# Kernel tuning notes

Hardware: AMD Instinct MI355X
Metric: run time of the kernel (lower is better)

## Reference

```python
import jax, jax.numpy as jnp
import numpy as np

B, S, H, DK = 4, 2048, 16, 64
D = H * DK  # d_model = 1024


def setup_inputs() -> dict:
    key = jax.random.key(0)
    ks = jax.random.split(key, 11)
    s = 1.0 / np.sqrt(D)
    return {
        "query": jax.random.normal(ks[0], (B, S, D), dtype=jnp.float32),
        "value": jax.random.normal(ks[1], (B, S, D), dtype=jnp.float32),
        "key": jax.random.normal(ks[2], (B, S, D), dtype=jnp.float32),
        "Wq": jax.random.normal(ks[3], (D, D), dtype=jnp.float32) * s,
        "bq": jnp.zeros((D,), dtype=jnp.float32),
        "Wk": jax.random.normal(ks[4], (D, D), dtype=jnp.float32) * s,
        "bk": jnp.zeros((D,), dtype=jnp.float32),
        "Wv": jax.random.normal(ks[5], (D, D), dtype=jnp.float32) * s,
        "bv": jnp.zeros((D,), dtype=jnp.float32),
        "Wo": jax.random.normal(ks[6], (D, D), dtype=jnp.float32) * s,
        "bo": jnp.zeros((D,), dtype=jnp.float32),
    }


def _split_heads(x):
    # [B, S, D] -> [B, H, S, DK]
    return x.reshape(B, -1, H, DK).transpose(0, 2, 1, 3)


def reference(query, value, key, Wq, bq, Wk, bk, Wv, bv, Wo, bo):
    q = _split_heads(query @ Wq + bq)
    k = _split_heads(key @ Wk + bk)
    v = _split_heads(value @ Wv + bv)
    logits = jnp.einsum("bhqd,bhkd->bhqk", q, k) / jnp.sqrt(jnp.float32(DK))
    attn = jax.nn.softmax(logits, axis=-1)
    out = jnp.einsum("bhqk,bhkd->bhqd", attn, v)  # [B, H, S, DK]
    out = out.transpose(0, 2, 1, 3).reshape(B, -1, D)
    return out @ Wo + bo
```

## Files before the change

### kernel.cpp

```cpp
#include <hip/hip_runtime.h>

typedef unsigned short u16;
typedef __attribute__((ext_vector_type(4))) short short4v;
typedef __attribute__((ext_vector_type(8))) short short8;
typedef __attribute__((ext_vector_type(4))) float f32x4;

#define MB_ (1024 * 1024)

__device__ __forceinline__ u16 f2bf(float f) {
  union { float f; unsigned int u; } v; v.f = f;
  unsigned int r = (v.u + 0x7FFFu + ((v.u >> 16) & 1u)) >> 16;
  return (u16)r;
}

__device__ __forceinline__ unsigned int pkbf(float a, float b) {
  union { float f; unsigned int u; } x, y; x.f = a; y.f = b;
  return __builtin_amdgcn_perm(y.u + 0x8000u, x.u + 0x8000u, 0x07060302u);
}

__device__ __forceinline__ void async16(const void* g, void* l) {
  __builtin_amdgcn_global_load_lds((__attribute__((address_space(1))) void*)g,
                                   (__attribute__((address_space(3))) void*)l, 16, 0, 0);
}

__device__ __forceinline__ f32x4 mfma32(short8 a, short8 b, f32x4 c) {
  return __builtin_amdgcn_mfma_f32_16x16x32_bf16(a, b, c, 0, 0, 0);
}

__global__ void cvt_x(const float* __restrict__ a, const float* __restrict__ b,
                      const float* __restrict__ c, u16* __restrict__ oa,
                      u16* __restrict__ ob, u16* __restrict__ oc) {
  const float* s = blockIdx.y == 0 ? a : (blockIdx.y == 1 ? b : c);
  u16* d = blockIdx.y == 0 ? oa : (blockIdx.y == 1 ? ob : oc);
  size_t i = ((size_t)blockIdx.x * 256 + threadIdx.x) * 4;
  float4 f = *(const float4*)&s[i];
  ushort4 o;
  o.x = f2bf(f.x); o.y = f2bf(f.y); o.z = f2bf(f.z); o.w = f2bf(f.w);
  *(ushort4*)&d[i] = o;
}

__global__ void wtrans(const float* __restrict__ w0, const float* __restrict__ w1,
                       const float* __restrict__ w2, const float* __restrict__ w3,
                       u16* __restrict__ o0, u16* __restrict__ o1,
                       u16* __restrict__ o2, u16* __restrict__ o3) {
  const int z = blockIdx.z;
  const float* in = z == 0 ? w0 : (z == 1 ? w1 : (z == 2 ? w2 : w3));
  u16* out = z == 0 ? o0 : (z == 1 ? o1 : (z == 2 ? o2 : o3));
  __shared__ float tile[32][33];
  const int bx = blockIdx.x * 32, by = blockIdx.y * 32;
  for (int i = threadIdx.y; i < 32; i += 8)
    tile[i][threadIdx.x] = in[(size_t)(by + i) * 1024 + bx + threadIdx.x];
  __syncthreads();
  for (int i = threadIdx.y; i < 32; i += 8)
    out[(size_t)(bx + i) * 1024 + by + threadIdx.x] = f2bf(tile[threadIdx.x][i]);
}

__device__ __forceinline__ void gemm_body(const u16* __restrict__ A, const u16* __restrict__ Bt,
                                          const float* __restrict__ bias, float alpha,
                                          int mode, void* __restrict__ outp) {
  __shared__ __align__(16) u16 As[128 * 32];
  __shared__ __align__(16) u16 Bs[128 * 32];
  const int t = threadIdx.x, wave = t >> 6, lane = t & 63;
  const int m0 = blockIdx.y * 128, n0 = blockIdx.x * 128;
  const int wm = (wave >> 1) * 64, wn = (wave & 1) * 64;
  const int lrow = lane >> 2, lcol = (lane & 3) * 8;
  f32x4 acc[4][4] = {};
  for (int k0 = 0; k0 < 1024; k0 += 32) {
    __syncthreads();
#pragma unroll
    for (int c = 0; c < 2; ++c) {
      const int chunk = wave * 2 + c;
      const int row = chunk * 16 + lrow;
      async16(&A[(size_t)(m0 + row) * 1024 + k0 + lcol], &As[chunk * 512]);
      async16(&Bt[(size_t)(n0 + row) * 1024 + k0 + lcol], &Bs[chunk * 512]);
    }
    __syncthreads();
    short8 af[4], bf[4];
#pragma unroll
    for (int mb = 0; mb < 4; ++mb)
      af[mb] = *(const short8*)&As[(wm + mb * 16 + (lane & 15)) * 32 + (lane >> 4) * 8];
#pragma unroll
    for (int nb = 0; nb < 4; ++nb)
      bf[nb] = *(const short8*)&Bs[(wn + nb * 16 + (lane & 15)) * 32 + (lane >> 4) * 8];
#pragma unroll
    for (int mb = 0; mb < 4; ++mb)
#pragma unroll
      for (int nb = 0; nb < 4; ++nb)
        acc[mb][nb] = mfma32(af[mb], bf[nb], acc[mb][nb]);
  }
#pragma unroll
  for (int mb = 0; mb < 4; ++mb)
#pragma unroll
    for (int nb = 0; nb < 4; ++nb) {
      const int n = n0 + wn + nb * 16 + (lane & 15);
      const float bn = bias[n];
      if (mode == 2) {
        const int h = n >> 6, d = n & 63;
        const int mbase = m0 + wm + mb * 16 + (lane >> 4) * 4;
        const int b = mbase >> 11, s = mbase & 2047;
        union { unsigned int u[2]; ushort4 s4; } pk;
        pk.u[0] = pkbf(acc[mb][nb][0] + bn, acc[mb][nb][1] + bn);
        pk.u[1] = pkbf(acc[mb][nb][2] + bn, acc[mb][nb][3] + bn);
        *(ushort4*)&((u16*)outp)[(size_t)((b * 16 + h) * 64 + d) * 2048 + s] = pk.s4;
      } else if (mode == 1) {
#pragma unroll
        for (int r = 0; r < 4; ++r) {
          const int m = m0 + wm + mb * 16 + (lane >> 4) * 4 + r;
          const int b = m >> 11, s = m & 2047, h = n >> 6, d = n & 63;
          ((u16*)outp)[(size_t)((b * 16 + h) * 2048 + s) * 64 + d] =
              f2bf(acc[mb][nb][r] * alpha + bn * alpha);
        }
      } else {
#pragma unroll
        for (int r = 0; r < 4; ++r) {
          const int m = m0 + wm + mb * 16 + (lane >> 4) * 4 + r;
          ((float*)outp)[(size_t)m * 1024 + n] = acc[mb][nb][r] + bn;
        }
      }
    }
}

__global__ __launch_bounds__(256, 3) void gemm_proj(
    const u16* xq, const u16* xk, const u16* xv,
    const u16* wq, const u16* wk, const u16* wv,
    const float* bq, const float* bk, const float* bv,
    u16* oq, u16* ok, u16* ov, float aq) {
  const int z = blockIdx.z;
  const u16* A = z == 0 ? xq : (z == 1 ? xk : xv);
  const u16* B = z == 0 ? wq : (z == 1 ? wk : wv);
  const float* bi = z == 0 ? bq : (z == 1 ? bk : bv);
  void* o = z == 0 ? (void*)oq : (z == 1 ? (void*)ok : (void*)ov);
  gemm_body(A, B, bi, z == 0 ? aq : 1.0f, z == 2 ? 2 : 1, o);
}

__global__ __launch_bounds__(256, 3) void gemm_out(const u16* A, const u16* Bt,
                                                   const float* bias, float* o) {
  gemm_body(A, Bt, bias, 1.0f, 0, o);
}

__global__ __launch_bounds__(256, 4) void flash_attn(const u16* __restrict__ Q,
                                                     const u16* __restrict__ K,
                                                     const u16* __restrict__ Vt,
                                                     u16* __restrict__ O) {
  __shared__ __align__(16) u16 lds[2 * 64 * 64];
  u16* Ks = lds;
  u16* Vs = lds + 4096;
  const int t = threadIdx.x, wave = t >> 6, lane = t & 63;
  const int quad = lane >> 4, q15 = lane & 15, sw = q15 & 7;
  const int bh = blockIdx.y, q0 = blockIdx.x * 64;
  const u16* Qb = Q + (size_t)bh * 2048 * 64;
  const u16* Kb = K + (size_t)bh * 2048 * 64;
  const u16* Vb = Vt + (size_t)bh * 64 * 2048;
  const int qr = q0 + wave * 16 + q15;
  const short8 qf0 = *(const short8*)&Qb[(size_t)qr * 64 + quad * 8];
  const short8 qf1 = *(const short8*)&Qb[(size_t)qr * 64 + 32 + quad * 8];
  f32x4 oacc[4] = {};
  float l = 0.f;
  for (int kc = 0; kc < 2048; kc += 64) {
    __syncthreads();
#pragma unroll
    for (int c = 0; c < 2; ++c) {
      const int i = wave * 2 + c;
      const int row = i * 8 + (lane >> 3);
      const int ch = (lane & 7) ^ (row & 7);
      async16(&Kb[(size_t)(kc + row) * 64 + ch * 8], &Ks[i * 512]);
      async16(&Vb[(size_t)row * 2048 + kc + ch * 8], &Vs[i * 512]);
    }
    __syncthreads();
    short4v pk[4];
#pragma unroll
    for (int ma = 0; ma < 4; ++ma) {
      const int rowo = (ma * 16 + q15) * 64;
      const short8 k0 = *(const short8*)&Ks[rowo + ((quad ^ sw) * 8)];
      const short8 k1 = *(const short8*)&Ks[rowo + (((4 + quad) ^ sw) * 8)];
      f32x4 s0 = {};
      s0 = mfma32(k0, qf0, s0);
      s0 = mfma32(k1, qf1, s0);
      float p0 = __builtin_exp2f(s0[0]);
      float p1 = __builtin_exp2f(s0[1]);
      float p2 = __builtin_exp2f(s0[2]);
      float p3 = __builtin_exp2f(s0[3]);
      l += (p0 + p1) + (p2 + p3);
      union { unsigned int u[2]; short4v s4; } pq;
      pq.u[0] = pkbf(p0, p1);
      pq.u[1] = pkbf(p2, p3);
      pk[ma] = pq.s4;
    }
#if __has_builtin(__builtin_amdgcn_mfma_f32_16x16x16bf16_1k)
#pragma unroll
    for (int mb = 0; mb < 4; ++mb) {
      const int vrow = (mb * 16 + q15) * 64;
#pragma unroll
      for (int kb = 0; kb < 4; ++kb) {
        const int pos = (((kb * 2 + (quad >> 1)) ^ sw) * 8) + (quad & 1) * 4;
        const short4v vf = *(const short4v*)&Vs[vrow + pos];
        oacc[mb] = __builtin_amdgcn_mfma_f32_16x16x16bf16_1k(vf, pk[kb], oacc[mb], 0, 0, 0);
      }
    }
#else
    {
      const int* pi = (const int*)&pk[0];
#pragma unroll
      for (int kb2 = 0; kb2 < 2; ++kb2) {
        const int lo = quad < 2 ? pi[kb2 * 4 + 0] : pi[kb2 * 4 + 2];
        const int hi = quad < 2 ? pi[kb2 * 4 + 1] : pi[kb2 * 4 + 3];
        const int src = (2 * (quad & 1)) * 16 + q15;
        union { int i[4]; short8 s; } u;
        u.i[0] = __shfl(lo, src);      u.i[1] = __shfl(hi, src);
        u.i[2] = __shfl(lo, src + 16); u.i[3] = __shfl(hi, src + 16);
#pragma unroll
        for (int mb = 0; mb < 4; ++mb) {
          const short8 vf8 = *(const short8*)&Vs[(mb * 16 + q15) * 64 + (((kb2 * 4 + quad) ^ sw) * 8)];
          oacc[mb] = mfma32(vf8, u.s, oacc[mb]);
        }
      }
    }
#endif
  }
  l += __shfl_xor(l, 16);
  l += __shfl_xor(l, 32);
  const float inv = 1.f / l;
  __syncthreads();
  u16* Es = lds + wave * 1024;
#pragma unroll
  for (int mb = 0; mb < 4; ++mb) {
    const int posc = ((mb * 2 + (quad >> 1)) ^ sw) * 8 + (quad & 1) * 4;
    union { unsigned int u[2]; ushort4 s4; } pq;
    pq.u[0] = pkbf(oacc[mb][0] * inv, oacc[mb][1] * inv);
    pq.u[1] = pkbf(oacc[mb][2] * inv, oacc[mb][3] * inv);
    *(ushort4*)&Es[q15 * 64 + posc] = pq.s4;
  }
  const int b = bh >> 4, h = bh & 15;
#pragma unroll
  for (int pass = 0; pass < 2; ++pass) {
    const int rw = pass * 8 + (lane >> 3);
    const int j = lane & 7;
    const short8 val = *(const short8*)&Es[rw * 64 + ((j ^ (rw & 7)) * 8)];
    *(short8*)&O[((size_t)(b * 2048 + q0 + wave * 16 + rw)) * 1024 + h * 64 + j * 8] = val;
  }
}

extern "C" void kernel_launch(void* const* d_in, const int* in_sizes, int n_in,
                              void* d_out, int out_size, void* d_ws, size_t ws_size,
                              hipStream_t stream) {
  const float* q_in = (const float*)d_in[0];
  const float* v_in = (const float*)d_in[1];
  const float* k_in = (const float*)d_in[2];
  const float* Wq = (const float*)d_in[3];
  const float* bq = (const float*)d_in[4];
  const float* Wk = (const float*)d_in[5];
  const float* bk = (const float*)d_in[6];
  const float* Wv = (const float*)d_in[7];
  const float* bv = (const float*)d_in[8];
  const float* Wo = (const float*)d_in[9];
  const float* bo = (const float*)d_in[10];
  float* out = (float*)d_out;
  char* ws = (char*)d_ws;

  u16* xq = (u16*)(ws);
  u16* xk = (u16*)(ws + 16 * (size_t)MB_);
  u16* xv = (u16*)(ws + 32 * (size_t)MB_);
  u16* wqT = (u16*)(ws + 48 * (size_t)MB_);
  u16* wkT = (u16*)(ws + 50 * (size_t)MB_);
  u16* wvT = (u16*)(ws + 52 * (size_t)MB_);
  u16* woT = (u16*)(ws + 54 * (size_t)MB_);
  u16* qb = (u16*)(ws + 56 * (size_t)MB_);
  u16* kb = (u16*)(ws + 72 * (size_t)MB_);
  u16* vb = (u16*)(ws + 88 * (size_t)MB_);
  u16* ao = xq;

  const float aq = 0.125f * 1.44269504088896340736f;

  cvt_x<<<dim3(8192, 3), 256, 0, stream>>>(q_in, k_in, v_in, xq, xk, xv);
  wtrans<<<dim3(32, 32, 4), dim3(32, 8), 0, stream>>>(Wq, Wk, Wv, Wo, wqT, wkT, wvT, woT);
  gemm_proj<<<dim3(8, 64, 3), 256, 0, stream>>>(xq, xk, xv, wqT, wkT, wvT, bq, bk, bv, qb, kb, vb, aq);
  flash_attn<<<dim3(32, 64), 256, 0, stream>>>(qb, kb, vb, ao);
  gemm_out<<<dim3(8, 64), 256, 0, stream>>>(ao, woT, bo, out);
}
```

Before: 392.9 us.

## Double-buffer K/V tiles in flash attention with async prefetch

The flash attention loop now stages the next K/V tile into a second LDS buffer while the current tile is computed, using vmcnt waits and raw barriers instead of two syncthreads per iteration. The aim is to hide global-to-LDS load latency behind the MFMA and exp work. It also swaps the manual bf16 packing for the hardware v_cvt_pk_bf16_f32 instruction and raises launch bounds occupancy to 5. The cost is doubled LDS per block (32KB), which may cap how many blocks fit per CU, and the vmcnt counting must match the number of outstanding async loads.

```diff
diff --git a/kernel.cpp b/kernel.cpp
--- a/kernel.cpp
+++ b/kernel.cpp
@@ -16,6 +16,12 @@
 __device__ __forceinline__ unsigned int pkbf(float a, float b) {
   union { float f; unsigned int u; } x, y; x.f = a; y.f = b;
   return __builtin_amdgcn_perm(y.u + 0x8000u, x.u + 0x8000u, 0x07060302u);
+}
+
+__device__ __forceinline__ unsigned int cvtpk(float a, float b) {
+  unsigned int r;
+  asm("v_cvt_pk_bf16_f32 %0, %1, %2" : "=v"(r) : "v"(a), "v"(b));
+  return r;
 }
 
 __device__ __forceinline__ void async16(const void* g, void* l) {
@@ -138,13 +144,11 @@
   gemm_body(A, Bt, bias, 1.0f, 0, o);
 }
 
-__global__ __launch_bounds__(256, 4) void flash_attn(const u16* __restrict__ Q,
+__global__ __launch_bounds__(256, 5) void flash_attn(const u16* __restrict__ Q,
                                                      const u16* __restrict__ K,
                                                      const u16* __restrict__ Vt,
                                                      u16* __restrict__ O) {
-  __shared__ __align__(16) u16 lds[2 * 64 * 64];
-  u16* Ks = lds;
-  u16* Vs = lds + 4096;
+  __shared__ __align__(16) u16 lds[2 * 2 * 64 * 64];
   const int t = threadIdx.x, wave = t >> 6, lane = t & 63;
   const int quad = lane >> 4, q15 = lane & 15, sw = q15 & 7;
   const int bh = blockIdx.y, q0 = blockIdx.x * 64;
@@ -156,17 +160,33 @@
   const short8 qf1 = *(const short8*)&Qb[(size_t)qr * 64 + 32 + quad * 8];
   f32x4 oacc[4] = {};
   float l = 0.f;
-  for (int kc = 0; kc < 2048; kc += 64) {
-    __syncthreads();
+
+  auto stage = [&](int kc, int buf) {
+    u16* Ksb = lds + buf * 8192;
+    u16* Vsb = Ksb + 4096;
 #pragma unroll
     for (int c = 0; c < 2; ++c) {
       const int i = wave * 2 + c;
       const int row = i * 8 + (lane >> 3);
       const int ch = (lane & 7) ^ (row & 7);
-      async16(&Kb[(size_t)(kc + row) * 64 + ch * 8], &Ks[i * 512]);
-      async16(&Vb[(size_t)row * 2048 + kc + ch * 8], &Vs[i * 512]);
-    }
-    __syncthreads();
+      async16(&Kb[(size_t)(kc + row) * 64 + ch * 8], &Ksb[i * 512]);
+      async16(&Vb[(size_t)row * 2048 + kc + ch * 8], &Vsb[i * 512]);
+    }
+  };
+
+  stage(0, 0);
+  for (int tk = 0; tk < 32; ++tk) {
+    const int buf = tk & 1;
+    if (tk < 31) {
+      stage((tk + 1) * 64, buf ^ 1);
+      asm volatile("s_waitcnt vmcnt(4)" ::: "memory");
+    } else {
+      asm volatile("s_waitcnt vmcnt(0)" ::: "memory");
+    }
+    __builtin_amdgcn_s_barrier();
+    asm volatile("" ::: "memory");
+    const u16* Ks = lds + buf * 8192;
+    const u16* Vs = Ks + 4096;
     short4v pk[4];
 #pragma unroll
     for (int ma = 0; ma < 4; ++ma) {
@@ -182,8 +202,8 @@
       float p3 = __builtin_exp2f(s0[3]);
       l += (p0 + p1) + (p2 + p3);
       union { unsigned int u[2]; short4v s4; } pq;
-      pq.u[0] = pkbf(p0, p1);
-      pq.u[1] = pkbf(p2, p3);
+      pq.u[0] = cvtpk(p0, p1);
+      pq.u[1] = cvtpk(p2, p3);
       pk[ma] = pq.s4;
     }
 #if __has_builtin(__builtin_amdgcn_mfma_f32_16x16x16bf16_1k)
@@ -216,6 +236,8 @@
       }
     }
 #endif
+    asm volatile("" ::: "memory");
+    __builtin_amdgcn_s_barrier();
   }
   l += __shfl_xor(l, 16);
   l += __shfl_xor(l, 32);
@@ -226,8 +248,8 @@
   for (int mb = 0; mb < 4; ++mb) {
     const int posc = ((mb * 2 + (quad >> 1)) ^ sw) * 8 + (quad & 1) * 4;
     union { unsigned int u[2]; ushort4 s4; } pq;
-    pq.u[0] = pkbf(oacc[mb][0] * inv, oacc[mb][1] * inv);
-    pq.u[1] = pkbf(oacc[mb][2] * inv, oacc[mb][3] * inv);
+    pq.u[0] = cvtpk(oacc[mb][0] * inv, oacc[mb][1] * inv);
+    pq.u[1] = cvtpk(oacc[mb][2] * inv, oacc[mb][3] * inv);
     *(ushort4*)&Es[q15 * 64 + posc] = pq.s4;
   }
   const int b = bh >> 4, h = bh & 15;
```

Result: no change. 389.3 us (-0.9%).
